# Optimization experiments

Hardware: AMD Instinct MI355X
Metric: run time of the kernel (lower is better)

## Reference

```python
import jax, jax.numpy as jnp
import numpy as np

BSZ, SEQLEN, DIM = 2, 2048, 4096
N_HEADS, N_KV_HEADS, HEAD_DIM = 32, 8, 128
N_REP = N_HEADS // N_KV_HEADS
MAX_SEQ_LEN = 2048
ROPE_THETA = 500000.0
NEG_INF = -1e9


def setup_inputs() -> dict:
    key = jax.random.key(0)
    ks = jax.random.split(key, 6)
    scale = 0.02
    x = jax.random.normal(ks[0], (BSZ, SEQLEN, DIM), dtype=jnp.float32)
    wq = jax.random.normal(ks[1], (DIM, N_HEADS * HEAD_DIM), dtype=jnp.float32) * scale
    wk = jax.random.normal(ks[2], (DIM, N_KV_HEADS * HEAD_DIM), dtype=jnp.float32) * scale
    wv = jax.random.normal(ks[3], (DIM, N_KV_HEADS * HEAD_DIM), dtype=jnp.float32) * scale
    wo = jax.random.normal(ks[4], (N_HEADS * HEAD_DIM, DIM), dtype=jnp.float32) * scale
    # RoPE frequencies (llama precompute_freqs_cis)
    inv_freq = 1.0 / (ROPE_THETA ** (jnp.arange(0, HEAD_DIM, 2, dtype=jnp.float32) / HEAD_DIM))
    t = jnp.arange(SEQLEN, dtype=jnp.float32)
    freqs = jnp.outer(t, inv_freq)  # [seqlen, head_dim//2]
    freqs_cos = jnp.cos(freqs)
    freqs_sin = jnp.sin(freqs)
    # causal additive mask for prefill (start_pos=0)
    mask = jnp.triu(jnp.full((SEQLEN, SEQLEN), NEG_INF, dtype=jnp.float32), k=1)
    cache_k = jnp.zeros((BSZ, MAX_SEQ_LEN, N_KV_HEADS, HEAD_DIM), dtype=jnp.float32)
    cache_v = jnp.zeros((BSZ, MAX_SEQ_LEN, N_KV_HEADS, HEAD_DIM), dtype=jnp.float32)
    return {"x": x, "wq": wq, "wk": wk, "wv": wv, "wo": wo,
            "freqs_cos": freqs_cos, "freqs_sin": freqs_sin, "mask": mask,
            "cache_k": cache_k, "cache_v": cache_v, "start_pos": 0}


def apply_rotary_emb(x, cos, sin):
    # x: [b, s, h, d]; cos/sin: [s, d//2]
    x2 = x.reshape(*x.shape[:-1], -1, 2)
    xe, xo = x2[..., 0], x2[..., 1]
    c = cos[None, :, None, :]
    s = sin[None, :, None, :]
    oe = xe * c - xo * s
    oo = xe * s + xo * c
    return jnp.stack([oe, oo], axis=-1).reshape(x.shape)


def repeat_kv(x, n_rep):
    # [b, k, n_kv, d] -> [b, k, n_kv*n_rep, d]
    b, k, h, d = x.shape
    return jnp.broadcast_to(x[:, :, :, None, :], (b, k, h, n_rep, d)).reshape(b, k, h * n_rep, d)


def reference(x, wq, wk, wv, wo, freqs_cos, freqs_sin, mask, cache_k, cache_v, start_pos):
    bsz, seqlen, _ = x.shape
    xq = (x @ wq).reshape(bsz, seqlen, N_HEADS, HEAD_DIM)
    xk = (x @ wk).reshape(bsz, seqlen, N_KV_HEADS, HEAD_DIM)
    xv = (x @ wv).reshape(bsz, seqlen, N_KV_HEADS, HEAD_DIM)
    xq = apply_rotary_emb(xq, freqs_cos, freqs_sin)
    xk = apply_rotary_emb(xk, freqs_cos, freqs_sin)
    # KV-cache append
    cache_k = jax.lax.dynamic_update_slice(cache_k, xk, (0, start_pos, 0, 0))
    cache_v = jax.lax.dynamic_update_slice(cache_v, xv, (0, start_pos, 0, 0))
    kv_len = start_pos + seqlen
    keys = repeat_kv(cache_k[:, :kv_len], N_REP)      # [b, k, H, d]
    values = repeat_kv(cache_v[:, :kv_len], N_REP)
    q = xq.transpose(0, 2, 1, 3)                      # [b, H, s, d]
    k = keys.transpose(0, 2, 1, 3)
    v = values.transpose(0, 2, 1, 3)
    scores = jnp.einsum('bhsd,bhkd->bhsk', q, k) / jnp.sqrt(jnp.float32(HEAD_DIM))
    scores = scores + mask[None, None, :, :]
    probs = jax.nn.softmax(scores.astype(jnp.float32), axis=-1).astype(q.dtype)
    out = jnp.einsum('bhsk,bhkd->bhsd', probs, v)
    out = out.transpose(0, 2, 1, 3).reshape(bsz, seqlen, -1)
    return out @ wo
```

## Files before the change

### kernel.cpp

```cpp
#include <hip/hip_runtime.h>
#include <hip/hip_bf16.h>

typedef __bf16 bf16_t;
typedef __attribute__((ext_vector_type(4))) __bf16 bf16x4;
typedef __attribute__((ext_vector_type(8))) __bf16 bf16x8;
typedef __attribute__((ext_vector_type(4))) float f32x4;

#define DIM   4096
#define NQKV  6144
#define S_LEN 2048
#define HD    128

__device__ __forceinline__ void gload_lds16(const void* g, void* l) {
  __builtin_amdgcn_global_load_lds(
      (__attribute__((address_space(1))) void*)(g),
      (__attribute__((address_space(3))) void*)(l), 16, 0, 0);
}

__global__ __launch_bounds__(256) void convert_bf16(const float* __restrict__ src,
                                                    bf16_t* __restrict__ dst) {
  size_t i = ((size_t)blockIdx.x * 256 + threadIdx.x) * 8;
  f32x4 a = *(const f32x4*)(src + i);
  f32x4 b = *(const f32x4*)(src + i + 4);
  bf16x8 o;
#pragma unroll
  for (int j = 0; j < 4; ++j) { o[j] = (bf16_t)a[j]; o[4 + j] = (bf16_t)b[j]; }
  *(bf16x8*)(dst + i) = o;
}

__global__ __launch_bounds__(256) void transpose_all(const float* __restrict__ wq,
                                                     const float* __restrict__ wk,
                                                     const float* __restrict__ wv,
                                                     const float* __restrict__ wo,
                                                     bf16_t* __restrict__ wqkvT,
                                                     bf16_t* __restrict__ woT) {
  __shared__ float tile[64][65];
  int blk = blockIdx.x;
  const float* src; bf16_t* dst; int N, by, bx;
  if (blk < 4096)      { src = wq; dst = wqkvT;                        N = 4096; by = blk >> 6; bx = blk & 63; }
  else if (blk < 5120) { blk -= 4096; src = wk; dst = wqkvT + (size_t)4096 * 4096; N = 1024; by = blk >> 4; bx = blk & 15; }
  else if (blk < 6144) { blk -= 5120; src = wv; dst = wqkvT + (size_t)5120 * 4096; N = 1024; by = blk >> 4; bx = blk & 15; }
  else                 { blk -= 6144; src = wo; dst = woT;             N = 4096; by = blk >> 6; bx = blk & 63; }
  const int k0 = by * 64, n0 = bx * 64;
  const int t = threadIdx.x;
#pragma unroll
  for (int p = 0; p < 4; ++p) {
    int idx = p * 256 + t;
    int r = idx >> 4, c4 = (idx & 15) * 4;
    f32x4 v = *(const f32x4*)&src[(size_t)(k0 + r) * N + n0 + c4];
    tile[r][c4] = v[0]; tile[r][c4 + 1] = v[1];
    tile[r][c4 + 2] = v[2]; tile[r][c4 + 3] = v[3];
  }
  __syncthreads();
#pragma unroll
  for (int p = 0; p < 4; ++p) {
    int idx = p * 256 + t;
    int r = idx >> 4, c4 = (idx & 15) * 4;
    bf16x4 o;
    o[0] = (bf16_t)tile[c4][r];     o[1] = (bf16_t)tile[c4 + 1][r];
    o[2] = (bf16_t)tile[c4 + 2][r]; o[3] = (bf16_t)tile[c4 + 3][r];
    *(bf16x4*)&dst[(size_t)(n0 + r) * 4096 + k0 + c4] = o;
  }
}

template <typename CT, bool ROPE>
__global__ __launch_bounds__(512) void gemm256(const bf16_t* __restrict__ A,
                                               const bf16_t* __restrict__ Bt,
                                               CT* __restrict__ C,
                                               int ldc, int nbx, int col0,
                                               const float* __restrict__ cosT,
                                               const float* __restrict__ sinT) {
  __shared__ __align__(16) bf16_t As[32768];
  __shared__ __align__(16) bf16_t Bs[32768];
  const int tid  = threadIdx.x;
  const int lane = tid & 63;
  const int w    = tid >> 6;
  const int wm   = w >> 2, wn = w & 3;
  const int l15 = lane & 15, l4 = lane >> 4, l7 = lane & 7;

  const int cpx = gridDim.x >> 3;
  const int swz = (blockIdx.x & 7) * cpx + (blockIdx.x >> 3);
  const int by = swz / nbx, bx = swz - by * nbx;
  const int bm = by * 256, bn = bx * 256;

  const size_t g_off0 = (size_t)((w * 2 + 0) * 8 + (lane >> 3)) * 4096
                      + (((lane & 7) ^ ((lane >> 3) & 7)) * 8);
  const size_t g_off1 = g_off0 + (size_t)8 * 4096;
  const int l_off0 = (w * 2 + 0) * 512;
  const int l_off1 = (w * 2 + 1) * 512;

#define STAGE(gsrc, ldst) do { \
    gload_lds16((gsrc) + g_off0, (ldst) + l_off0); \
    gload_lds16((gsrc) + g_off1, (ldst) + l_off1); } while (0)

  const bf16_t* Ab = A  + (size_t)bm * 4096;
  const bf16_t* Bb = Bt + (size_t)bn * 4096;
  const size_t HLF = (size_t)128 * 4096;

  f32x4 acc[8][4];
#pragma unroll
  for (int i = 0; i < 8; ++i)
#pragma unroll
    for (int j = 0; j < 4; ++j) { f32x4 z = {0.f, 0.f, 0.f, 0.f}; acc[i][j] = z; }

  STAGE(Bb,             Bs);
  STAGE(Ab,             As);
  STAGE(Bb + HLF,       Bs + 8192);
  STAGE(Ab + HLF,       As + 8192);
  STAGE(Bb + 64,        Bs + 16384);
  STAGE(Ab + 64,        As + 16384);
  STAGE(Bb + HLF + 64,  Bs + 16384 + 8192);
  asm volatile("s_waitcnt vmcnt(6)" ::: "memory");
  __builtin_amdgcn_s_barrier();

  for (int t = 0; t < 64; ++t) {
    const int cu = t & 1;
    bf16_t* Ac = As + cu * 16384;
    bf16_t* Bc = Bs + cu * 16384;
    bf16_t* Axn = As + (cu ^ 1) * 16384;
    const bf16_t* A1g = Ab + (size_t)(t + 1) * 64;
    const bf16_t* A2g = Ab + (size_t)(t + 2) * 64;
    const bf16_t* B2g = Bb + (size_t)(t + 2) * 64;

    bf16x8 af[4][2], b0[2][2], b1[2][2];

#pragma unroll
    for (int f = 0; f < 4; ++f)
#pragma unroll
      for (int kh = 0; kh < 2; ++kh)
        af[f][kh] = *(const bf16x8*)&Ac[(wm * 64 + f * 16 + l15) * 64 + (((kh * 4 + l4) ^ l7) * 8)];
#pragma unroll
    for (int fb = 0; fb < 2; ++fb)
#pragma unroll
      for (int kh = 0; kh < 2; ++kh)
        b0[fb][kh] = *(const bf16x8*)&Bc[(wn * 32 + fb * 16 + l15) * 64 + (((kh * 4 + l4) ^ l7) * 8)];
    if (t + 1 < 64) STAGE(A1g + HLF, Axn + 8192);
    __builtin_amdgcn_s_barrier();
    asm volatile("s_waitcnt lgkmcnt(0)" ::: "memory");
    __builtin_amdgcn_sched_barrier(0);
    __builtin_amdgcn_s_setprio(1);
#pragma unroll
    for (int f = 0; f < 4; ++f)
#pragma unroll
      for (int fb = 0; fb < 2; ++fb)
#pragma unroll
        for (int kh = 0; kh < 2; ++kh)
          acc[f][fb] = __builtin_amdgcn_mfma_f32_16x16x32_bf16(af[f][kh], b0[fb][kh], acc[f][fb], 0, 0, 0);
    __builtin_amdgcn_s_setprio(0);
    __builtin_amdgcn_s_barrier();

#pragma unroll
    for (int fb = 0; fb < 2; ++fb)
#pragma unroll
      for (int kh = 0; kh < 2; ++kh)
        b1[fb][kh] = *(const bf16x8*)&Bc[8192 + (wn * 32 + fb * 16 + l15) * 64 + (((kh * 4 + l4) ^ l7) * 8)];
    if (t + 2 < 64) STAGE(B2g, Bc);
    __builtin_amdgcn_s_barrier();
    asm volatile("s_waitcnt lgkmcnt(0)" ::: "memory");
    __builtin_amdgcn_sched_barrier(0);
    __builtin_amdgcn_s_setprio(1);
#pragma unroll
    for (int f = 0; f < 4; ++f)
#pragma unroll
      for (int fb = 0; fb < 2; ++fb)
#pragma unroll
        for (int kh = 0; kh < 2; ++kh)
          acc[f][2 + fb] = __builtin_amdgcn_mfma_f32_16x16x32_bf16(af[f][kh], b1[fb][kh], acc[f][2 + fb], 0, 0, 0);
    __builtin_amdgcn_s_setprio(0);
    __builtin_amdgcn_s_barrier();

#pragma unroll
    for (int f = 0; f < 4; ++f)
#pragma unroll
      for (int kh = 0; kh < 2; ++kh)
        af[f][kh] = *(const bf16x8*)&Ac[8192 + (wm * 64 + f * 16 + l15) * 64 + (((kh * 4 + l4) ^ l7) * 8)];
    if (t + 2 < 64) STAGE(A2g, Ac);
    __builtin_amdgcn_s_barrier();
    asm volatile("s_waitcnt lgkmcnt(0)" ::: "memory");
    __builtin_amdgcn_sched_barrier(0);
    __builtin_amdgcn_s_setprio(1);
#pragma unroll
    for (int f = 0; f < 4; ++f)
#pragma unroll
      for (int fb = 0; fb < 2; ++fb)
#pragma unroll
        for (int kh = 0; kh < 2; ++kh)
          acc[4 + f][fb] = __builtin_amdgcn_mfma_f32_16x16x32_bf16(af[f][kh], b0[fb][kh], acc[4 + f][fb], 0, 0, 0);
    __builtin_amdgcn_s_setprio(0);
    __builtin_amdgcn_s_barrier();

    if (t + 2 < 64) STAGE(B2g + HLF, Bc + 8192);
    __builtin_amdgcn_s_barrier();
    __builtin_amdgcn_s_setprio(1);
#pragma unroll
    for (int f = 0; f < 4; ++f)
#pragma unroll
      for (int fb = 0; fb < 2; ++fb)
#pragma unroll
        for (int kh = 0; kh < 2; ++kh)
          acc[4 + f][2 + fb] = __builtin_amdgcn_mfma_f32_16x16x32_bf16(af[f][kh], b1[fb][kh], acc[4 + f][2 + fb], 0, 0, 0);
    __builtin_amdgcn_s_setprio(0);
    if (t < 62)       asm volatile("s_waitcnt vmcnt(6)" ::: "memory");
    else if (t == 62) asm volatile("s_waitcnt vmcnt(0)" ::: "memory");
    __builtin_amdgcn_s_barrier();
  }
#undef STAGE

#pragma unroll
  for (int mi = 0; mi < 8; ++mi) {
    int row0 = bm + (mi >> 2) * 128 + wm * 64 + (mi & 3) * 16 + l4 * 4;
#pragma unroll
    for (int ni = 0; ni < 4; ++ni) {
      int col = bn + (ni >> 1) * 128 + wn * 32 + (ni & 1) * 16 + l15;
      int gcol = col0 + col;
      if (ROPE && gcol < 5120) {
        const int i = (gcol & 127) >> 1;
        const float scl = (gcol < 4096) ? 0.12751745f : 1.0f;
#pragma unroll
        for (int r = 0; r < 4; ++r) {
          int srow = (row0 + r) & (S_LEN - 1);
          float c = cosT[srow * 64 + i] * scl;
          float s = sinT[srow * 64 + i] * scl;
          float a = acc[mi][ni][r];
          float p = __shfl_xor(a, 1);
          float o = (l15 & 1) ? (p * s + a * c) : (a * c - p * s);
          C[(size_t)(row0 + r) * ldc + gcol] = (CT)o;
        }
      } else {
#pragma unroll
        for (int r = 0; r < 4; ++r)
          C[(size_t)(row0 + r) * ldc + gcol] = (CT)acc[mi][ni][r];
      }
    }
  }
}

template <typename CT, bool ROPE>
__global__ __launch_bounds__(512) void gemm128(const bf16_t* __restrict__ A,
                                               const bf16_t* __restrict__ Bt,
                                               CT* __restrict__ C,
                                               int ldc, int nbx, int col0,
                                               const float* __restrict__ cosT,
                                               const float* __restrict__ sinT) {
  __shared__ __align__(16) bf16_t As[2][8192];
  __shared__ __align__(16) bf16_t Bs[2][16384];
  const int tid  = threadIdx.x;
  const int lane = tid & 63;
  const int w    = tid >> 6;
  const int wm   = w >> 2, wn = w & 3;
  const int l15 = lane & 15, l4 = lane >> 4, l7 = lane & 7;

  const int cpx = gridDim.x >> 3;
  const int swz = (blockIdx.x & 7) * cpx + (blockIdx.x >> 3);
  const int by = swz / nbx, bx = swz - by * nbx;
  const int bm = by * 128, bn = bx * 256;

  const size_t g_off0 = (size_t)((w * 2 + 0) * 8 + (lane >> 3)) * 4096
                      + (((lane & 7) ^ ((lane >> 3) & 7)) * 8);
  const size_t g_off1 = g_off0 + (size_t)8 * 4096;
  const int l_off0 = (w * 2 + 0) * 512;
  const int l_off1 = (w * 2 + 1) * 512;

#define STAGE(gsrc, ldst) do { \
    gload_lds16((gsrc) + g_off0, (ldst) + l_off0); \
    gload_lds16((gsrc) + g_off1, (ldst) + l_off1); } while (0)

  const bf16_t* Ab = A  + (size_t)bm * 4096;
  const bf16_t* Bb = Bt + (size_t)bn * 4096;
  const size_t HLF = (size_t)128 * 4096;

  f32x4 acc[4][4];
#pragma unroll
  for (int i = 0; i < 4; ++i)
#pragma unroll
    for (int j = 0; j < 4; ++j) { f32x4 z = {0.f, 0.f, 0.f, 0.f}; acc[i][j] = z; }

  STAGE(Ab,        &As[0][0]);
  STAGE(Bb,        &Bs[0][0]);
  STAGE(Bb + HLF,  &Bs[0][8192]);
  STAGE(Bb + 64,   &Bs[1][0]);
  asm volatile("s_waitcnt vmcnt(2)" ::: "memory");
  __builtin_amdgcn_s_barrier();

  for (int t = 0; t < 64; ++t) {
    const int cu = t & 1;
    const bf16_t* A1g = Ab + (size_t)(t + 1) * 64;
    const bf16_t* B1g = Bb + (size_t)(t + 1) * 64;
    const bf16_t* B2g = Bb + (size_t)(t + 2) * 64;

    bf16x8 af[4][2], bl[2][2], bh[2][2];

#pragma unroll
    for (int f = 0; f < 4; ++f)
#pragma unroll
      for (int kh = 0; kh < 2; ++kh)
        af[f][kh] = *(const bf16x8*)&As[cu][(wm * 64 + f * 16 + l15) * 64 + (((kh * 4 + l4) ^ l7) * 8)];
#pragma unroll
    for (int fb = 0; fb < 2; ++fb)
#pragma unroll
      for (int kh = 0; kh < 2; ++kh)
        bl[fb][kh] = *(const bf16x8*)&Bs[cu][(wn * 32 + fb * 16 + l15) * 64 + (((kh * 4 + l4) ^ l7) * 8)];
    if (t + 1 < 64) {
      STAGE(A1g,       &As[cu ^ 1][0]);
      STAGE(B1g + HLF, &Bs[cu ^ 1][8192]);
    }
    __builtin_amdgcn_s_barrier();
    asm volatile("s_waitcnt lgkmcnt(0)" ::: "memory");
    __builtin_amdgcn_sched_barrier(0);
    __builtin_amdgcn_s_setprio(1);
#pragma unroll
    for (int f = 0; f < 4; ++f)
#pragma unroll
      for (int fb = 0; fb < 2; ++fb)
#pragma unroll
        for (int kh = 0; kh < 2; ++kh)
          acc[f][fb] = __builtin_amdgcn_mfma_f32_16x16x32_bf16(af[f][kh], bl[fb][kh], acc[f][fb], 0, 0, 0);
    __builtin_amdgcn_s_setprio(0);
    __builtin_amdgcn_s_barrier();

#pragma unroll
    for (int fb = 0; fb < 2; ++fb)
#pragma unroll
      for (int kh = 0; kh < 2; ++kh)
        bh[fb][kh] = *(const bf16x8*)&Bs[cu][8192 + (wn * 32 + fb * 16 + l15) * 64 + (((kh * 4 + l4) ^ l7) * 8)];
    if (t + 2 < 64) STAGE(B2g, &Bs[cu][0]);
    __builtin_amdgcn_s_barrier();
    asm volatile("s_waitcnt lgkmcnt(0)" ::: "memory");
    __builtin_amdgcn_sched_barrier(0);
    __builtin_amdgcn_s_setprio(1);
#pragma unroll
    for (int f = 0; f < 4; ++f)
#pragma unroll
      for (int fb = 0; fb < 2; ++fb)
#pragma unroll
        for (int kh = 0; kh < 2; ++kh)
          acc[f][2 + fb] = __builtin_amdgcn_mfma_f32_16x16x32_bf16(af[f][kh], bh[fb][kh], acc[f][2 + fb], 0, 0, 0);
    __builtin_amdgcn_s_setprio(0);
    if (t + 2 < 64) asm volatile("s_waitcnt vmcnt(2)" ::: "memory");
    else            asm volatile("s_waitcnt vmcnt(0)" ::: "memory");
    __builtin_amdgcn_s_barrier();
  }
#undef STAGE

#pragma unroll
  for (int f = 0; f < 4; ++f) {
    int row0 = bm + wm * 64 + f * 16 + l4 * 4;
#pragma unroll
    for (int fb = 0; fb < 4; ++fb) {
      int col = bn + (fb >> 1) * 128 + wn * 32 + (fb & 1) * 16 + l15;
      int gcol = col0 + col;
      if (ROPE && gcol < 5120) {
        const int i = (gcol & 127) >> 1;
        const float scl = (gcol < 4096) ? 0.12751745f : 1.0f;
#pragma unroll
        for (int r = 0; r < 4; ++r) {
          int srow = (row0 + r) & (S_LEN - 1);
          float c = cosT[srow * 64 + i] * scl;
          float s = sinT[srow * 64 + i] * scl;
          float a = acc[f][fb][r];
          float p = __shfl_xor(a, 1);
          float o = (l15 & 1) ? (p * s + a * c) : (a * c - p * s);
          C[(size_t)(row0 + r) * ldc + gcol] = (CT)o;
        }
      } else {
#pragma unroll
        for (int r = 0; r < 4; ++r)
          C[(size_t)(row0 + r) * ldc + gcol] = (CT)acc[f][fb][r];
      }
    }
  }
}

__global__ __launch_bounds__(512) void attn_fwd(const bf16_t* __restrict__ qkv,
                                                bf16_t* __restrict__ out) {
  const int pr = blockIdx.x;
  const int h  = blockIdx.y;
  const int b  = blockIdx.z;
  const int kvh = h >> 2;
  const int tid = threadIdx.x;
  const int w    = tid >> 6;
  const int lane = tid & 63;
  const int qloc = lane & 15;
  const int g    = lane >> 4;

  __shared__ __align__(16) bf16_t Ks[2][64 * 128];
  __shared__ __align__(16) bf16_t Vt[128 * 64];

  const bf16_t* kvbase = qkv + (size_t)b * S_LEN * NQKV + DIM + kvh * HD;
  const int vrow_t = tid >> 4;
  const int vcol_t = (tid & 15) * 8;

  const float M2 = 11.5415603f;
  bf16x8 ones8;
#pragma unroll
  for (int j = 0; j < 8; ++j) ones8[j] = (bf16_t)1.0f;

#pragma unroll 1
  for (int half = 0; half < 2; ++half) {
    const int qt = half ? pr : 7 - pr;
    const int W = qt * 256 + w * 32;
    const int nt = 4 * qt + 4;

    bf16x8 aq[2][4];
#pragma unroll
    for (int qb = 0; qb < 2; ++qb) {
      const bf16_t* qptr = qkv + (size_t)(b * S_LEN + W + qb * 16 + qloc) * NQKV + h * HD + g * 8;
#pragma unroll
      for (int c = 0; c < 4; ++c) aq[qb][c] = *(const bf16x8*)(qptr + c * 32);
    }

    f32x4 oacc[2][8];
    f32x4 lacc[2];
#pragma unroll
    for (int qb = 0; qb < 2; ++qb) {
#pragma unroll
      for (int d = 0; d < 8; ++d) { f32x4 z = {0.f, 0.f, 0.f, 0.f}; oacc[qb][d] = z; }
      f32x4 z = {0.f, 0.f, 0.f, 0.f}; lacc[qb] = z;
    }

    bf16x8 vreg[2];
#pragma unroll
    for (int p = 0; p < 2; ++p) {
      int chunk = p * 8 + w;
      int krow = chunk * 4 + g;
      int key = (krow & 3) | (((krow >> 3) & 1) << 2);
      gload_lds16(kvbase + (size_t)krow * NQKV + ((qloc ^ key) * 8), &Ks[0][chunk * 512]);
    }
#pragma unroll
    for (int p = 0; p < 2; ++p)
      vreg[p] = *(const bf16x8*)(kvbase + 1024 + (size_t)(p * 32 + vrow_t) * NQKV + vcol_t);

#pragma unroll 1
    for (int t = 0; t < nt; ++t) {
      const int kv0 = t * 64;
      const int cur = t & 1;

      if (t + 1 < nt) {
        const int kvn = kv0 + 64;
#pragma unroll
        for (int p = 0; p < 2; ++p) {
          int chunk = p * 8 + w;
          int krow = chunk * 4 + g;
          int key = (krow & 3) | (((krow >> 3) & 1) << 2);
          gload_lds16(kvbase + (size_t)(kvn + krow) * NQKV + ((qloc ^ key) * 8),
                      &Ks[cur ^ 1][chunk * 512]);
        }
        asm volatile("s_waitcnt vmcnt(2)" ::: "memory");
      } else {
        asm volatile("s_waitcnt vmcnt(0)" ::: "memory");
      }

#pragma unroll
      for (int p = 0; p < 2; ++p) {
        int vrow = p * 32 + vrow_t;
        int rk = (vrow >> 3) ^ (tid & 7);
#pragma unroll
        for (int j = 0; j < 8; ++j)
          Vt[(vcol_t + j) * 64 + ((rk ^ j) * 8) + (vrow & 7)] = vreg[p][j];
      }
      if (t + 1 < nt) {
        const int kvn = kv0 + 64;
#pragma unroll
        for (int p = 0; p < 2; ++p)
          vreg[p] = *(const bf16x8*)(kvbase + 1024 + (size_t)(kvn + p * 32 + vrow_t) * NQKV + vcol_t);
      }
      asm volatile("s_waitcnt lgkmcnt(0)" ::: "memory");
      __builtin_amdgcn_s_barrier();

      if (kv0 <= W + 31) {
        f32x4 sacc[2][2][2];
#pragma unroll
        for (int qb = 0; qb < 2; ++qb)
#pragma unroll
          for (int w2 = 0; w2 < 2; ++w2)
#pragma unroll
            for (int hf = 0; hf < 2; ++hf) { f32x4 z = {0.f, 0.f, 0.f, 0.f}; sacc[qb][w2][hf] = z; }
#pragma unroll
        for (int w2 = 0; w2 < 2; ++w2)
#pragma unroll
          for (int hf = 0; hf < 2; ++hf) {
            int r = 32 * w2 + 8 * (qloc >> 2) + 4 * hf + (qloc & 3);
            int key = (r & 3) | (((r >> 3) & 1) << 2);
            bf16x8 bk[4];
#pragma unroll
            for (int c = 0; c < 4; ++c)
              bk[c] = *(const bf16x8*)&Ks[cur][r * 128 + (((c * 4 + g) ^ key) * 8)];
            __builtin_amdgcn_s_setprio(1);
#pragma unroll
            for (int qb = 0; qb < 2; ++qb)
#pragma unroll
              for (int c = 0; c < 4; ++c)
                sacc[qb][w2][hf] = __builtin_amdgcn_mfma_f32_16x16x32_bf16(bk[c], aq[qb][c], sacc[qb][w2][hf], 0, 0, 0);
            __builtin_amdgcn_s_setprio(0);
          }

        const bool diag = (kv0 + 63 > W);
        bf16x8 pa[2][2];
#pragma unroll
        for (int qb = 0; qb < 2; ++qb) {
          const int qg = W + qb * 16 + qloc;
#pragma unroll
          for (int w2 = 0; w2 < 2; ++w2)
#pragma unroll
            for (int hf = 0; hf < 2; ++hf)
#pragma unroll
              for (int r = 0; r < 4; ++r) {
                float e = exp2f(sacc[qb][w2][hf][r] - M2);
                if (diag) {
                  int kg = kv0 + 32 * w2 + 8 * g + 4 * hf + r;
                  e = (kg <= qg) ? e : 0.f;
                }
                pa[qb][w2][hf * 4 + r] = (bf16_t)e;
              }
        }

#pragma unroll
        for (int w2 = 0; w2 < 2; ++w2)
#pragma unroll
          for (int dt = 0; dt < 8; ++dt) {
            int d = dt * 16 + qloc;
            int key2 = (4 * w2 + g) ^ (d & 7) ^ ((d >> 3) & 7);
            bf16x8 bv = *(const bf16x8*)&Vt[d * 64 + key2 * 8];
            __builtin_amdgcn_s_setprio(1);
#pragma unroll
            for (int qb = 0; qb < 2; ++qb)
              oacc[qb][dt] = __builtin_amdgcn_mfma_f32_16x16x32_bf16(bv, pa[qb][w2], oacc[qb][dt], 0, 0, 0);
            __builtin_amdgcn_s_setprio(0);
          }
        __builtin_amdgcn_s_setprio(1);
#pragma unroll
        for (int w2 = 0; w2 < 2; ++w2)
#pragma unroll
          for (int qb = 0; qb < 2; ++qb)
            lacc[qb] = __builtin_amdgcn_mfma_f32_16x16x32_bf16(ones8, pa[qb][w2], lacc[qb], 0, 0, 0);
        __builtin_amdgcn_s_setprio(0);
      }
      __builtin_amdgcn_s_barrier();
    }

#pragma unroll
    for (int qb = 0; qb < 2; ++qb) {
      float inv = 1.f / lacc[qb][0];
      bf16_t* op = out + (size_t)(b * S_LEN + W + qb * 16 + qloc) * DIM + h * HD;
#pragma unroll
      for (int dt = 0; dt < 8; ++dt) {
        bf16x4 o4;
#pragma unroll
        for (int r = 0; r < 4; ++r) o4[r] = (bf16_t)(oacc[qb][dt][r] * inv);
        *(bf16x4*)(op + dt * 16 + 4 * g) = o4;
      }
    }
  }
}

extern "C" void kernel_launch(void* const* d_in, const int* in_sizes, int n_in,
                              void* d_out, int out_size, void* d_ws, size_t ws_size,
                              hipStream_t stream) {
  const float* x  = (const float*)d_in[0];
  const float* wq = (const float*)d_in[1];
  const float* wk = (const float*)d_in[2];
  const float* wv = (const float*)d_in[3];
  const float* wo = (const float*)d_in[4];
  const float* fc = (const float*)d_in[5];
  const float* fs = (const float*)d_in[6];

  bf16_t* ws    = (bf16_t*)d_ws;
  bf16_t* wqkvT = ws;
  bf16_t* woT   = wqkvT + (size_t)6144 * 4096;
  bf16_t* qkv   = woT   + (size_t)4096 * 4096;
  bf16_t* xb    = qkv   + (size_t)4096 * 6144;
  bf16_t* ao    = xb;

  convert_bf16<<<8192, 256, 0, stream>>>(x, xb);
  transpose_all<<<10240, 256, 0, stream>>>(wq, wk, wv, wo, wqkvT, woT);

  gemm256<bf16_t, true><<<256, 512, 0, stream>>>(xb, wqkvT, qkv, 6144, 16, 0, fc, fs);
  gemm128<bf16_t, true><<<256, 512, 0, stream>>>(xb, wqkvT + (size_t)4096 * 4096, qkv,
                                                 6144, 8, 4096, fc, fs);
  attn_fwd<<<dim3(4, 32, 2), 512, 0, stream>>>(qkv, ao);
  gemm256<float, false><<<256, 512, 0, stream>>>(ao, woT, (float*)d_out, 4096, 16, 0, nullptr, nullptr);
}
```

Baseline: 493.3 us.

## Enlarge attention KV tile to 128, sum softmax denominators in registers, drop GEMM waits

```diff
diff --git a/kernel.cpp b/kernel.cpp
--- a/kernel.cpp
+++ b/kernel.cpp
@@ -136,8 +136,6 @@
         b0[fb][kh] = *(const bf16x8*)&Bc[(wn * 32 + fb * 16 + l15) * 64 + (((kh * 4 + l4) ^ l7) * 8)];
     if (t + 1 < 64) STAGE(A1g + HLF, Axn + 8192);
     __builtin_amdgcn_s_barrier();
-    asm volatile("s_waitcnt lgkmcnt(0)" ::: "memory");
-    __builtin_amdgcn_sched_barrier(0);
     __builtin_amdgcn_s_setprio(1);
 #pragma unroll
     for (int f = 0; f < 4; ++f)
@@ -156,8 +154,6 @@
         b1[fb][kh] = *(const bf16x8*)&Bc[8192 + (wn * 32 + fb * 16 + l15) * 64 + (((kh * 4 + l4) ^ l7) * 8)];
     if (t + 2 < 64) STAGE(B2g, Bc);
     __builtin_amdgcn_s_barrier();
-    asm volatile("s_waitcnt lgkmcnt(0)" ::: "memory");
-    __builtin_amdgcn_sched_barrier(0);
     __builtin_amdgcn_s_setprio(1);
 #pragma unroll
     for (int f = 0; f < 4; ++f)
@@ -176,8 +172,6 @@
         af[f][kh] = *(const bf16x8*)&Ac[8192 + (wm * 64 + f * 16 + l15) * 64 + (((kh * 4 + l4) ^ l7) * 8)];
     if (t + 2 < 64) STAGE(A2g, Ac);
     __builtin_amdgcn_s_barrier();
-    asm volatile("s_waitcnt lgkmcnt(0)" ::: "memory");
-    __builtin_amdgcn_sched_barrier(0);
     __builtin_amdgcn_s_setprio(1);
 #pragma unroll
     for (int f = 0; f < 4; ++f)
@@ -305,8 +299,6 @@
       STAGE(B1g + HLF, &Bs[cu ^ 1][8192]);
     }
     __builtin_amdgcn_s_barrier();
-    asm volatile("s_waitcnt lgkmcnt(0)" ::: "memory");
-    __builtin_amdgcn_sched_barrier(0);
     __builtin_amdgcn_s_setprio(1);
 #pragma unroll
     for (int f = 0; f < 4; ++f)
@@ -325,8 +317,6 @@
         bh[fb][kh] = *(const bf16x8*)&Bs[cu][8192 + (wn * 32 + fb * 16 + l15) * 64 + (((kh * 4 + l4) ^ l7) * 8)];
     if (t + 2 < 64) STAGE(B2g, &Bs[cu][0]);
     __builtin_amdgcn_s_barrier();
-    asm volatile("s_waitcnt lgkmcnt(0)" ::: "memory");
-    __builtin_amdgcn_sched_barrier(0);
     __builtin_amdgcn_s_setprio(1);
 #pragma unroll
     for (int f = 0; f < 4; ++f)
@@ -383,23 +373,20 @@
   const int qloc = lane & 15;
   const int g    = lane >> 4;
 
-  __shared__ __align__(16) bf16_t Ks[2][64 * 128];
-  __shared__ __align__(16) bf16_t Vt[128 * 64];
+  __shared__ __align__(16) bf16_t Ks[2][128 * 128];
+  __shared__ __align__(16) bf16_t Vt[128 * 128];
 
   const bf16_t* kvbase = qkv + (size_t)b * S_LEN * NQKV + DIM + kvh * HD;
   const int vrow_t = tid >> 4;
   const int vcol_t = (tid & 15) * 8;
 
   const float M2 = 11.5415603f;
-  bf16x8 ones8;
-#pragma unroll
-  for (int j = 0; j < 8; ++j) ones8[j] = (bf16_t)1.0f;
 
 #pragma unroll 1
   for (int half = 0; half < 2; ++half) {
     const int qt = half ? pr : 7 - pr;
     const int W = qt * 256 + w * 32;
-    const int nt = 4 * qt + 4;
+    const int nt = 2 * qt + 2;
 
     bf16x8 aq[2][4];
 #pragma unroll
@@ -410,137 +397,139 @@
     }
 
     f32x4 oacc[2][8];
-    f32x4 lacc[2];
-#pragma unroll
-    for (int qb = 0; qb < 2; ++qb) {
+    float lsum[2] = {0.f, 0.f};
+#pragma unroll
+    for (int qb = 0; qb < 2; ++qb)
 #pragma unroll
       for (int d = 0; d < 8; ++d) { f32x4 z = {0.f, 0.f, 0.f, 0.f}; oacc[qb][d] = z; }
-      f32x4 z = {0.f, 0.f, 0.f, 0.f}; lacc[qb] = z;
-    }
-
-    bf16x8 vreg[2];
-#pragma unroll
-    for (int p = 0; p < 2; ++p) {
+
+    bf16x8 vreg[4];
+#pragma unroll
+    for (int p = 0; p < 4; ++p) {
       int chunk = p * 8 + w;
       int krow = chunk * 4 + g;
       int key = (krow & 3) | (((krow >> 3) & 1) << 2);
       gload_lds16(kvbase + (size_t)krow * NQKV + ((qloc ^ key) * 8), &Ks[0][chunk * 512]);
     }
 #pragma unroll
-    for (int p = 0; p < 2; ++p)
+    for (int p = 0; p < 4; ++p)
       vreg[p] = *(const bf16x8*)(kvbase + 1024 + (size_t)(p * 32 + vrow_t) * NQKV + vcol_t);
 
 #pragma unroll 1
     for (int t = 0; t < nt; ++t) {
-      const int kv0 = t * 64;
+      const int kv0 = t * 128;
       const int cur = t & 1;
 
       if (t + 1 < nt) {
-        const int kvn = kv0 + 64;
-#pragma unroll
-        for (int p = 0; p < 2; ++p) {
+        const int kvn = kv0 + 128;
+#pragma unroll
+        for (int p = 0; p < 4; ++p) {
           int chunk = p * 8 + w;
           int krow = chunk * 4 + g;
           int key = (krow & 3) | (((krow >> 3) & 1) << 2);
           gload_lds16(kvbase + (size_t)(kvn + krow) * NQKV + ((qloc ^ key) * 8),
                       &Ks[cur ^ 1][chunk * 512]);
         }
-        asm volatile("s_waitcnt vmcnt(2)" ::: "memory");
+        asm volatile("s_waitcnt vmcnt(4)" ::: "memory");
       } else {
         asm volatile("s_waitcnt vmcnt(0)" ::: "memory");
       }
 
 #pragma unroll
-      for (int p = 0; p < 2; ++p) {
+      for (int p = 0; p < 4; ++p) {
         int vrow = p * 32 + vrow_t;
         int rk = (vrow >> 3) ^ (tid & 7);
 #pragma unroll
         for (int j = 0; j < 8; ++j)
-          Vt[(vcol_t + j) * 64 + ((rk ^ j) * 8) + (vrow & 7)] = vreg[p][j];
+          Vt[(vcol_t + j) * 128 + ((rk ^ j) * 8) + (vrow & 7)] = vreg[p][j];
       }
       if (t + 1 < nt) {
-        const int kvn = kv0 + 64;
-#pragma unroll
-        for (int p = 0; p < 2; ++p)
+        const int kvn = kv0 + 128;
+#pragma unroll
+        for (int p = 0; p < 4; ++p)
           vreg[p] = *(const bf16x8*)(kvbase + 1024 + (size_t)(kvn + p * 32 + vrow_t) * NQKV + vcol_t);
       }
       asm volatile("s_waitcnt lgkmcnt(0)" ::: "memory");
       __builtin_amdgcn_s_barrier();
 
       if (kv0 <= W + 31) {
-        f32x4 sacc[2][2][2];
-#pragma unroll
-        for (int qb = 0; qb < 2; ++qb)
-#pragma unroll
-          for (int w2 = 0; w2 < 2; ++w2)
-#pragma unroll
-            for (int hf = 0; hf < 2; ++hf) { f32x4 z = {0.f, 0.f, 0.f, 0.f}; sacc[qb][w2][hf] = z; }
-#pragma unroll
-        for (int w2 = 0; w2 < 2; ++w2)
-#pragma unroll
-          for (int hf = 0; hf < 2; ++hf) {
-            int r = 32 * w2 + 8 * (qloc >> 2) + 4 * hf + (qloc & 3);
-            int key = (r & 3) | (((r >> 3) & 1) << 2);
-            bf16x8 bk[4];
-#pragma unroll
-            for (int c = 0; c < 4; ++c)
-              bk[c] = *(const bf16x8*)&Ks[cur][r * 128 + (((c * 4 + g) ^ key) * 8)];
-            __builtin_amdgcn_s_setprio(1);
+        const bool diag = (kv0 + 127 > W);
+#pragma unroll
+        for (int w2g = 0; w2g < 2; ++w2g) {
+          if (kv0 + 64 * w2g <= W + 31) {
+            f32x4 sacc[2][2][2];
 #pragma unroll
             for (int qb = 0; qb < 2; ++qb)
 #pragma unroll
-              for (int c = 0; c < 4; ++c)
-                sacc[qb][w2][hf] = __builtin_amdgcn_mfma_f32_16x16x32_bf16(bk[c], aq[qb][c], sacc[qb][w2][hf], 0, 0, 0);
-            __builtin_amdgcn_s_setprio(0);
+              for (int w2l = 0; w2l < 2; ++w2l)
+#pragma unroll
+                for (int hf = 0; hf < 2; ++hf) { f32x4 z = {0.f, 0.f, 0.f, 0.f}; sacc[qb][w2l][hf] = z; }
+#pragma unroll
+            for (int w2l = 0; w2l < 2; ++w2l)
+#pragma unroll
+              for (int hf = 0; hf < 2; ++hf) {
+                int w2 = 2 * w2g + w2l;
+                int rr = 32 * w2 + 8 * (qloc >> 2) + 4 * hf + (qloc & 3);
+                int key = (rr & 3) | (((rr >> 3) & 1) << 2);
+                bf16x8 bk[4];
+#pragma unroll
+                for (int c = 0; c < 4; ++c)
+                  bk[c] = *(const bf16x8*)&Ks[cur][rr * 128 + (((c * 4 + g) ^ key) * 8)];
+                __builtin_amdgcn_s_setprio(1);
+#pragma unroll
+                for (int qb = 0; qb < 2; ++qb)
+#pragma unroll
+                  for (int c = 0; c < 4; ++c)
+                    sacc[qb][w2l][hf] = __builtin_amdgcn_mfma_f32_16x16x32_bf16(bk[c], aq[qb][c], sacc[qb][w2l][hf], 0, 0, 0);
+                __builtin_amdgcn_s_setprio(0);
+              }
+
+            bf16x8 pa[2][2];
+#pragma unroll
+            for (int qb = 0; qb < 2; ++qb) {
+              const int qg = W + qb * 16 + qloc;
+#pragma unroll
+              for (int w2l = 0; w2l < 2; ++w2l)
+#pragma unroll
+                for (int hf = 0; hf < 2; ++hf)
+#pragma unroll
+                  for (int r = 0; r < 4; ++r) {
+                    float e = exp2f(sacc[qb][w2l][hf][r] - M2);
+                    if (diag) {
+                      int kg = kv0 + 32 * (2 * w2g + w2l) + 8 * g + 4 * hf + r;
+                      e = (kg <= qg) ? e : 0.f;
+                    }
+                    lsum[qb] += e;
+                    pa[qb][w2l][hf * 4 + r] = (bf16_t)e;
+                  }
+            }
+
+#pragma unroll
+            for (int w2l = 0; w2l < 2; ++w2l)
+#pragma unroll
+              for (int dt = 0; dt < 8; ++dt) {
+                int w2 = 2 * w2g + w2l;
+                int d = dt * 16 + qloc;
+                int key2 = (4 * w2 + g) ^ (d & 7) ^ ((d >> 3) & 7);
+                bf16x8 bv = *(const bf16x8*)&Vt[d * 128 + key2 * 8];
+                __builtin_amdgcn_s_setprio(1);
+#pragma unroll
+                for (int qb = 0; qb < 2; ++qb)
+                  oacc[qb][dt] = __builtin_amdgcn_mfma_f32_16x16x32_bf16(bv, pa[qb][w2l], oacc[qb][dt], 0, 0, 0);
+                __builtin_amdgcn_s_setprio(0);
+              }
           }
-
-        const bool diag = (kv0 + 63 > W);
-        bf16x8 pa[2][2];
-#pragma unroll
-        for (int qb = 0; qb < 2; ++qb) {
-          const int qg = W + qb * 16 + qloc;
-#pragma unroll
-          for (int w2 = 0; w2 < 2; ++w2)
-#pragma unroll
-            for (int hf = 0; hf < 2; ++hf)
-#pragma unroll
-              for (int r = 0; r < 4; ++r) {
-                float e = exp2f(sacc[qb][w2][hf][r] - M2);
-                if (diag) {
-                  int kg = kv0 + 32 * w2 + 8 * g + 4 * hf + r;
-                  e = (kg <= qg) ? e : 0.f;
-                }
-                pa[qb][w2][hf * 4 + r] = (bf16_t)e;
-              }
         }
-
-#pragma unroll
-        for (int w2 = 0; w2 < 2; ++w2)
-#pragma unroll
-          for (int dt = 0; dt < 8; ++dt) {
-            int d = dt * 16 + qloc;
-            int key2 = (4 * w2 + g) ^ (d & 7) ^ ((d >> 3) & 7);
-            bf16x8 bv = *(const bf16x8*)&Vt[d * 64 + key2 * 8];
-            __builtin_amdgcn_s_setprio(1);
-#pragma unroll
-            for (int qb = 0; qb < 2; ++qb)
-              oacc[qb][dt] = __builtin_amdgcn_mfma_f32_16x16x32_bf16(bv, pa[qb][w2], oacc[qb][dt], 0, 0, 0);
-            __builtin_amdgcn_s_setprio(0);
-          }
-        __builtin_amdgcn_s_setprio(1);
-#pragma unroll
-        for (int w2 = 0; w2 < 2; ++w2)
-#pragma unroll
-          for (int qb = 0; qb < 2; ++qb)
-            lacc[qb] = __builtin_amdgcn_mfma_f32_16x16x32_bf16(ones8, pa[qb][w2], lacc[qb], 0, 0, 0);
-        __builtin_amdgcn_s_setprio(0);
       }
       __builtin_amdgcn_s_barrier();
     }
 
 #pragma unroll
     for (int qb = 0; qb < 2; ++qb) {
-      float inv = 1.f / lacc[qb][0];
+      float ls = lsum[qb];
+      ls += __shfl_xor(ls, 16);
+      ls += __shfl_xor(ls, 32);
+      float inv = 1.f / ls;
       bf16_t* op = out + (size_t)(b * S_LEN + W + qb * 16 + qloc) * DIM + h * HD;
 #pragma unroll
       for (int dt = 0; dt < 8; ++dt) {
```

New measurement: 491.4 us, median of 2. Within noise of the previous version (-0.4%).

## Split attention into one query tile per block and compute row sums on VALU

Applied to the files above, without the earlier changes.

```diff
diff --git a/kernel.cpp b/kernel.cpp
--- a/kernel.cpp
+++ b/kernel.cpp
@@ -136,8 +136,6 @@
         b0[fb][kh] = *(const bf16x8*)&Bc[(wn * 32 + fb * 16 + l15) * 64 + (((kh * 4 + l4) ^ l7) * 8)];
     if (t + 1 < 64) STAGE(A1g + HLF, Axn + 8192);
     __builtin_amdgcn_s_barrier();
-    asm volatile("s_waitcnt lgkmcnt(0)" ::: "memory");
-    __builtin_amdgcn_sched_barrier(0);
     __builtin_amdgcn_s_setprio(1);
 #pragma unroll
     for (int f = 0; f < 4; ++f)
@@ -156,8 +154,6 @@
         b1[fb][kh] = *(const bf16x8*)&Bc[8192 + (wn * 32 + fb * 16 + l15) * 64 + (((kh * 4 + l4) ^ l7) * 8)];
     if (t + 2 < 64) STAGE(B2g, Bc);
     __builtin_amdgcn_s_barrier();
-    asm volatile("s_waitcnt lgkmcnt(0)" ::: "memory");
-    __builtin_amdgcn_sched_barrier(0);
     __builtin_amdgcn_s_setprio(1);
 #pragma unroll
     for (int f = 0; f < 4; ++f)
@@ -176,8 +172,6 @@
         af[f][kh] = *(const bf16x8*)&Ac[8192 + (wm * 64 + f * 16 + l15) * 64 + (((kh * 4 + l4) ^ l7) * 8)];
     if (t + 2 < 64) STAGE(A2g, Ac);
     __builtin_amdgcn_s_barrier();
-    asm volatile("s_waitcnt lgkmcnt(0)" ::: "memory");
-    __builtin_amdgcn_sched_barrier(0);
     __builtin_amdgcn_s_setprio(1);
 #pragma unroll
     for (int f = 0; f < 4; ++f)
@@ -305,8 +299,6 @@
       STAGE(B1g + HLF, &Bs[cu ^ 1][8192]);
     }
     __builtin_amdgcn_s_barrier();
-    asm volatile("s_waitcnt lgkmcnt(0)" ::: "memory");
-    __builtin_amdgcn_sched_barrier(0);
     __builtin_amdgcn_s_setprio(1);
 #pragma unroll
     for (int f = 0; f < 4; ++f)
@@ -325,8 +317,6 @@
         bh[fb][kh] = *(const bf16x8*)&Bs[cu][8192 + (wn * 32 + fb * 16 + l15) * 64 + (((kh * 4 + l4) ^ l7) * 8)];
     if (t + 2 < 64) STAGE(B2g, &Bs[cu][0]);
     __builtin_amdgcn_s_barrier();
-    asm volatile("s_waitcnt lgkmcnt(0)" ::: "memory");
-    __builtin_amdgcn_sched_barrier(0);
     __builtin_amdgcn_s_setprio(1);
 #pragma unroll
     for (int f = 0; f < 4; ++f)
@@ -373,7 +363,8 @@
 
 __global__ __launch_bounds__(512) void attn_fwd(const bf16_t* __restrict__ qkv,
                                                 bf16_t* __restrict__ out) {
-  const int pr = blockIdx.x;
+  const int qtmap[8] = {7, 0, 6, 1, 5, 2, 4, 3};
+  const int qt = qtmap[blockIdx.x & 7];
   const int h  = blockIdx.y;
   const int b  = blockIdx.z;
   const int kvh = h >> 2;
@@ -391,164 +382,151 @@
   const int vcol_t = (tid & 15) * 8;
 
   const float M2 = 11.5415603f;
-  bf16x8 ones8;
-#pragma unroll
-  for (int j = 0; j < 8; ++j) ones8[j] = (bf16_t)1.0f;
+  const int W = qt * 256 + w * 32;
+  const int nt = 4 * qt + 4;
+
+  bf16x8 aq[2][4];
+#pragma unroll
+  for (int qb = 0; qb < 2; ++qb) {
+    const bf16_t* qptr = qkv + (size_t)(b * S_LEN + W + qb * 16 + qloc) * NQKV + h * HD + g * 8;
+#pragma unroll
+    for (int c = 0; c < 4; ++c) aq[qb][c] = *(const bf16x8*)(qptr + c * 32);
+  }
+
+  f32x4 oacc[2][8];
+  float lsum[2] = {0.f, 0.f};
+#pragma unroll
+  for (int qb = 0; qb < 2; ++qb)
+#pragma unroll
+    for (int d = 0; d < 8; ++d) { f32x4 z = {0.f, 0.f, 0.f, 0.f}; oacc[qb][d] = z; }
+
+  bf16x8 vreg[2];
+#pragma unroll
+  for (int p = 0; p < 2; ++p) {
+    int chunk = p * 8 + w;
+    int krow = chunk * 4 + g;
+    int key = (krow & 3) | (((krow >> 3) & 1) << 2);
+    gload_lds16(kvbase + (size_t)krow * NQKV + ((qloc ^ key) * 8), &Ks[0][chunk * 512]);
+  }
+#pragma unroll
+  for (int p = 0; p < 2; ++p)
+    vreg[p] = *(const bf16x8*)(kvbase + 1024 + (size_t)(p * 32 + vrow_t) * NQKV + vcol_t);
 
 #pragma unroll 1
-  for (int half = 0; half < 2; ++half) {
-    const int qt = half ? pr : 7 - pr;
-    const int W = qt * 256 + w * 32;
-    const int nt = 4 * qt + 4;
-
-    bf16x8 aq[2][4];
-#pragma unroll
-    for (int qb = 0; qb < 2; ++qb) {
-      const bf16_t* qptr = qkv + (size_t)(b * S_LEN + W + qb * 16 + qloc) * NQKV + h * HD + g * 8;
-#pragma unroll
-      for (int c = 0; c < 4; ++c) aq[qb][c] = *(const bf16x8*)(qptr + c * 32);
-    }
-
-    f32x4 oacc[2][8];
-    f32x4 lacc[2];
-#pragma unroll
-    for (int qb = 0; qb < 2; ++qb) {
-#pragma unroll
-      for (int d = 0; d < 8; ++d) { f32x4 z = {0.f, 0.f, 0.f, 0.f}; oacc[qb][d] = z; }
-      f32x4 z = {0.f, 0.f, 0.f, 0.f}; lacc[qb] = z;
-    }
-
-    bf16x8 vreg[2];
+  for (int t = 0; t < nt; ++t) {
+    const int kv0 = t * 64;
+    const int cur = t & 1;
+
+    if (t + 1 < nt) {
+      const int kvn = kv0 + 64;
+#pragma unroll
+      for (int p = 0; p < 2; ++p) {
+        int chunk = p * 8 + w;
+        int krow = chunk * 4 + g;
+        int key = (krow & 3) | (((krow >> 3) & 1) << 2);
+        gload_lds16(kvbase + (size_t)(kvn + krow) * NQKV + ((qloc ^ key) * 8),
+                    &Ks[cur ^ 1][chunk * 512]);
+      }
+      asm volatile("s_waitcnt vmcnt(2)" ::: "memory");
+    } else {
+      asm volatile("s_waitcnt vmcnt(0)" ::: "memory");
+    }
+
 #pragma unroll
     for (int p = 0; p < 2; ++p) {
-      int chunk = p * 8 + w;
-      int krow = chunk * 4 + g;
-      int key = (krow & 3) | (((krow >> 3) & 1) << 2);
-      gload_lds16(kvbase + (size_t)krow * NQKV + ((qloc ^ key) * 8), &Ks[0][chunk * 512]);
-    }
-#pragma unroll
-    for (int p = 0; p < 2; ++p)
-      vreg[p] = *(const bf16x8*)(kvbase + 1024 + (size_t)(p * 32 + vrow_t) * NQKV + vcol_t);
-
-#pragma unroll 1
-    for (int t = 0; t < nt; ++t) {
-      const int kv0 = t * 64;
-      const int cur = t & 1;
-
-      if (t + 1 < nt) {
-        const int kvn = kv0 + 64;
-#pragma unroll
-        for (int p = 0; p < 2; ++p) {
-          int chunk = p * 8 + w;
-          int krow = chunk * 4 + g;
-          int key = (krow & 3) | (((krow >> 3) & 1) << 2);
-          gload_lds16(kvbase + (size_t)(kvn + krow) * NQKV + ((qloc ^ key) * 8),
-                      &Ks[cur ^ 1][chunk * 512]);
+      int vrow = p * 32 + vrow_t;
+      int rk = (vrow >> 3) ^ (tid & 7);
+#pragma unroll
+      for (int j = 0; j < 8; ++j)
+        Vt[(vcol_t + j) * 64 + ((rk ^ j) * 8) + (vrow & 7)] = vreg[p][j];
+    }
+    if (t + 1 < nt) {
+      const int kvn = kv0 + 64;
+#pragma unroll
+      for (int p = 0; p < 2; ++p)
+        vreg[p] = *(const bf16x8*)(kvbase + 1024 + (size_t)(kvn + p * 32 + vrow_t) * NQKV + vcol_t);
+    }
+    asm volatile("s_waitcnt lgkmcnt(0)" ::: "memory");
+    __builtin_amdgcn_s_barrier();
+
+    if (kv0 <= W + 31) {
+      f32x4 sacc[2][2][2];
+#pragma unroll
+      for (int qb = 0; qb < 2; ++qb)
+#pragma unroll
+        for (int w2 = 0; w2 < 2; ++w2)
+#pragma unroll
+          for (int hf = 0; hf < 2; ++hf) { f32x4 z = {0.f, 0.f, 0.f, 0.f}; sacc[qb][w2][hf] = z; }
+#pragma unroll
+      for (int w2 = 0; w2 < 2; ++w2)
+#pragma unroll
+        for (int hf = 0; hf < 2; ++hf) {
+          int r = 32 * w2 + 8 * (qloc >> 2) + 4 * hf + (qloc & 3);
+          int key = (r & 3) | (((r >> 3) & 1) << 2);
+          bf16x8 bk[4];
+#pragma unroll
+          for (int c = 0; c < 4; ++c)
+            bk[c] = *(const bf16x8*)&Ks[cur][r * 128 + (((c * 4 + g) ^ key) * 8)];
+          __builtin_amdgcn_s_setprio(1);
+#pragma unroll
+          for (int qb = 0; qb < 2; ++qb)
+#pragma unroll
+            for (int c = 0; c < 4; ++c)
+              sacc[qb][w2][hf] = __builtin_amdgcn_mfma_f32_16x16x32_bf16(bk[c], aq[qb][c], sacc[qb][w2][hf], 0, 0, 0);
+          __builtin_amdgcn_s_setprio(0);
         }
-        asm volatile("s_waitcnt vmcnt(2)" ::: "memory");
-      } else {
-        asm volatile("s_waitcnt vmcnt(0)" ::: "memory");
+
+      const bool diag = (kv0 + 63 > W);
+      bf16x8 pa[2][2];
+#pragma unroll
+      for (int qb = 0; qb < 2; ++qb) {
+        const int qg = W + qb * 16 + qloc;
+#pragma unroll
+        for (int w2 = 0; w2 < 2; ++w2)
+#pragma unroll
+          for (int hf = 0; hf < 2; ++hf)
+#pragma unroll
+            for (int r = 0; r < 4; ++r) {
+              float e = exp2f(sacc[qb][w2][hf][r] - M2);
+              if (diag) {
+                int kg = kv0 + 32 * w2 + 8 * g + 4 * hf + r;
+                e = (kg <= qg) ? e : 0.f;
+              }
+              lsum[qb] += e;
+              pa[qb][w2][hf * 4 + r] = (bf16_t)e;
+            }
       }
 
 #pragma unroll
-      for (int p = 0; p < 2; ++p) {
-        int vrow = p * 32 + vrow_t;
-        int rk = (vrow >> 3) ^ (tid & 7);
-#pragma unroll
-        for (int j = 0; j < 8; ++j)
-          Vt[(vcol_t + j) * 64 + ((rk ^ j) * 8) + (vrow & 7)] = vreg[p][j];
-      }
-      if (t + 1 < nt) {
-        const int kvn = kv0 + 64;
-#pragma unroll
-        for (int p = 0; p < 2; ++p)
-          vreg[p] = *(const bf16x8*)(kvbase + 1024 + (size_t)(kvn + p * 32 + vrow_t) * NQKV + vcol_t);
-      }
-      asm volatile("s_waitcnt lgkmcnt(0)" ::: "memory");
-      __builtin_amdgcn_s_barrier();
-
-      if (kv0 <= W + 31) {
-        f32x4 sacc[2][2][2];
-#pragma unroll
-        for (int qb = 0; qb < 2; ++qb)
-#pragma unroll
-          for (int w2 = 0; w2 < 2; ++w2)
-#pragma unroll
-            for (int hf = 0; hf < 2; ++hf) { f32x4 z = {0.f, 0.f, 0.f, 0.f}; sacc[qb][w2][hf] = z; }
-#pragma unroll
-        for (int w2 = 0; w2 < 2; ++w2)
-#pragma unroll
-          for (int hf = 0; hf < 2; ++hf) {
-            int r = 32 * w2 + 8 * (qloc >> 2) + 4 * hf + (qloc & 3);
-            int key = (r & 3) | (((r >> 3) & 1) << 2);
-            bf16x8 bk[4];
-#pragma unroll
-            for (int c = 0; c < 4; ++c)
-              bk[c] = *(const bf16x8*)&Ks[cur][r * 128 + (((c * 4 + g) ^ key) * 8)];
-            __builtin_amdgcn_s_setprio(1);
-#pragma unroll
-            for (int qb = 0; qb < 2; ++qb)
-#pragma unroll
-              for (int c = 0; c < 4; ++c)
-                sacc[qb][w2][hf] = __builtin_amdgcn_mfma_f32_16x16x32_bf16(bk[c], aq[qb][c], sacc[qb][w2][hf], 0, 0, 0);
-            __builtin_amdgcn_s_setprio(0);
-          }
-
-        const bool diag = (kv0 + 63 > W);
-        bf16x8 pa[2][2];
-#pragma unroll
-        for (int qb = 0; qb < 2; ++qb) {
-          const int qg = W + qb * 16 + qloc;
-#pragma unroll
-          for (int w2 = 0; w2 < 2; ++w2)
-#pragma unroll
-            for (int hf = 0; hf < 2; ++hf)
-#pragma unroll
-              for (int r = 0; r < 4; ++r) {
-                float e = exp2f(sacc[qb][w2][hf][r] - M2);
-                if (diag) {
-                  int kg = kv0 + 32 * w2 + 8 * g + 4 * hf + r;
-                  e = (kg <= qg) ? e : 0.f;
-                }
-                pa[qb][w2][hf * 4 + r] = (bf16_t)e;
-              }
+      for (int w2 = 0; w2 < 2; ++w2)
+#pragma unroll
+        for (int dt = 0; dt < 8; ++dt) {
+          int d = dt * 16 + qloc;
+          int key2 = (4 * w2 + g) ^ (d & 7) ^ ((d >> 3) & 7);
+          bf16x8 bv = *(const bf16x8*)&Vt[d * 64 + key2 * 8];
+          __builtin_amdgcn_s_setprio(1);
+#pragma unroll
+          for (int qb = 0; qb < 2; ++qb)
+            oacc[qb][dt] = __builtin_amdgcn_mfma_f32_16x16x32_bf16(bv, pa[qb][w2], oacc[qb][dt], 0, 0, 0);
+          __builtin_amdgcn_s_setprio(0);
         }
-
-#pragma unroll
-        for (int w2 = 0; w2 < 2; ++w2)
-#pragma unroll
-          for (int dt = 0; dt < 8; ++dt) {
-            int d = dt * 16 + qloc;
-            int key2 = (4 * w2 + g) ^ (d & 7) ^ ((d >> 3) & 7);
-            bf16x8 bv = *(const bf16x8*)&Vt[d * 64 + key2 * 8];
-            __builtin_amdgcn_s_setprio(1);
-#pragma unroll
-            for (int qb = 0; qb < 2; ++qb)
-              oacc[qb][dt] = __builtin_amdgcn_mfma_f32_16x16x32_bf16(bv, pa[qb][w2], oacc[qb][dt], 0, 0, 0);
-            __builtin_amdgcn_s_setprio(0);
-          }
-        __builtin_amdgcn_s_setprio(1);
-#pragma unroll
-        for (int w2 = 0; w2 < 2; ++w2)
-#pragma unroll
-          for (int qb = 0; qb < 2; ++qb)
-            lacc[qb] = __builtin_amdgcn_mfma_f32_16x16x32_bf16(ones8, pa[qb][w2], lacc[qb], 0, 0, 0);
-        __builtin_amdgcn_s_setprio(0);
-      }
-      __builtin_amdgcn_s_barrier();
-    }
-
-#pragma unroll
-    for (int qb = 0; qb < 2; ++qb) {
-      float inv = 1.f / lacc[qb][0];
-      bf16_t* op = out + (size_t)(b * S_LEN + W + qb * 16 + qloc) * DIM + h * HD;
-#pragma unroll
-      for (int dt = 0; dt < 8; ++dt) {
-        bf16x4 o4;
-#pragma unroll
-        for (int r = 0; r < 4; ++r) o4[r] = (bf16_t)(oacc[qb][dt][r] * inv);
-        *(bf16x4*)(op + dt * 16 + 4 * g) = o4;
-      }
+    }
+    __builtin_amdgcn_s_barrier();
+  }
+
+#pragma unroll
+  for (int qb = 0; qb < 2; ++qb) {
+    float ls = lsum[qb];
+    ls += __shfl_xor(ls, 16);
+    ls += __shfl_xor(ls, 32);
+    float inv = 1.f / ls;
+    bf16_t* op = out + (size_t)(b * S_LEN + W + qb * 16 + qloc) * DIM + h * HD;
+#pragma unroll
+    for (int dt = 0; dt < 8; ++dt) {
+      bf16x4 o4;
+#pragma unroll
+      for (int r = 0; r < 4; ++r) o4[r] = (bf16_t)(oacc[qb][dt][r] * inv);
+      *(bf16x4*)(op + dt * 16 + 4 * g) = o4;
     }
   }
 }
@@ -577,6 +555,6 @@
   gemm256<bf16_t, true><<<256, 512, 0, stream>>>(xb, wqkvT, qkv, 6144, 16, 0, fc, fs);
   gemm128<bf16_t, true><<<256, 512, 0, stream>>>(xb, wqkvT + (size_t)4096 * 4096, qkv,
                                                  6144, 8, 4096, fc, fs);
-  attn_fwd<<<dim3(4, 32, 2), 512, 0, stream>>>(qkv, ao);
+  attn_fwd<<<dim3(8, 32, 2), 512, 0, stream>>>(qkv, ao);
   gemm256<float, false><<<256, 512, 0, stream>>>(ao, woT, (float*)d_out, 4096, 16, 0, nullptr, nullptr);
 }
```

New measurement: 577.4 us. +17.1%, slower.
